# Optimization experiments

Measured on AMD Instinct MI355X. Metric: run time of the kernel, lower is better.

## Reference

```python
import jax, jax.numpy as jnp
import numpy as np

T, H, V = 2048, 2048, 32000
NH, NKV, DH = 16, 4, 128
E, K, I = 16, 2, 1024
EPS = 1e-6
THETA = 1000000.0


def _rms(x, w):
    # RMSNorm with add_unit_offset: scale = (1 + w)
    v = jnp.mean(x * x, axis=-1, keepdims=True)
    return x * jax.lax.rsqrt(v + EPS) * (1.0 + w)


def _rope(x, pos):
    # x: [T, heads, DH], neox-style rotate-half RoPE
    inv = 1.0 / (THETA ** (jnp.arange(0, DH, 2, dtype=jnp.float32) / DH))
    ang = pos.astype(jnp.float32)[:, None] * inv[None, :]  # [T, DH/2]
    c, s = jnp.cos(ang)[:, None, :], jnp.sin(ang)[:, None, :]
    x1, x2 = x[..., : DH // 2], x[..., DH // 2 :]
    return jnp.concatenate([x1 * c - x2 * s, x2 * c + x1 * s], axis=-1)


def setup_inputs():
    key = jax.random.key(0)
    ks = jax.random.split(key, 12)

    def n(k, shp, scale=0.02):
        return jax.random.normal(k, shp, dtype=jnp.float32) * scale

    return {
        "input_ids": jax.random.randint(ks[0], (T,), 0, V),
        "positions": jnp.arange(T),
        "hidden_states": jax.random.normal(ks[1], (T, H), dtype=jnp.float32),
        "spec_step_idx": 0,
        "embed_w": n(ks[2], (V, H)),
        "fc_w": n(ks[3], (2 * H, H)),
        "pre_fc_emb_w": jnp.zeros((H,), jnp.float32),
        "pre_fc_hid_w": jnp.zeros((H,), jnp.float32),
        "in_ln_w": jnp.zeros((H,), jnp.float32),
        "post_ln_w": jnp.zeros((H,), jnp.float32),
        "final_norm_w": jnp.zeros((H,), jnp.float32),
        "wq": n(ks[4], (H, NH * DH)),
        "wk": n(ks[5], (H, NKV * DH)),
        "wv": n(ks[6], (H, NKV * DH)),
        "wo": n(ks[7], (NH * DH, H)),
        "q_norm_w": jnp.zeros((DH,), jnp.float32),
        "k_norm_w": jnp.zeros((DH,), jnp.float32),
        "router_w": n(ks[8], (H, E)),
        "w_gate": n(ks[9], (E, H, I)),
        "w_up": n(ks[10], (E, H, I)),
        "w_down": n(ks[11], (E, I, H)),
    }


def reference(input_ids, positions, hidden_states, spec_step_idx, embed_w, fc_w,
              pre_fc_emb_w, pre_fc_hid_w, in_ln_w, post_ln_w, final_norm_w,
              wq, wk, wv, wo, q_norm_w, k_norm_w, router_w, w_gate, w_up, w_down):
    # 1-3. embed -> pre_fc norms -> concat -> fc (2H -> H, no bias)
    emb = _rms(embed_w[input_ids], pre_fc_emb_w)
    hid = _rms(hidden_states, pre_fc_hid_w)
    x = jnp.concatenate([emb, hid], axis=-1) @ fc_w  # [T, H]

    # 4. decoder layer (layer_idx = spec_step_idx % 1 == 0); vLLM fused add-RMSNorm residual pattern
    residual = x
    x = _rms(x, in_ln_w)

    # GQA attention with per-head q/k RMSNorm + RoPE, causal
    q = _rms((x @ wq).reshape(T, NH, DH), q_norm_w)
    k = _rms((x @ wk).reshape(T, NKV, DH), k_norm_w)
    v = (x @ wv).reshape(T, NKV, DH)
    q, k = _rope(q, positions), _rope(k, positions)
    rep = NH // NKV
    k, v = jnp.repeat(k, rep, axis=1), jnp.repeat(v, rep, axis=1)  # [T, NH, DH]
    scores = jnp.einsum("qhd,khd->hqk", q, k) * (DH ** -0.5)
    causal = positions[:, None] >= positions[None, :]
    scores = jnp.where(causal[None], scores, jnp.float32(-1e30))
    attn = jax.nn.softmax(scores, axis=-1)
    x = jnp.einsum("hqk,khd->qhd", attn, v).reshape(T, NH * DH) @ wo

    # post-attention norm with fused residual add
    x = x + residual
    residual = x
    x = _rms(x, post_ln_w)

    # MoE: softmax router, top-k renormalized, SwiGLU experts (dense weighted combine)
    probs = jax.nn.softmax(x @ router_w, axis=-1)  # [T, E]
    topv, topi = jax.lax.top_k(probs, K)
    topv = topv / jnp.sum(topv, axis=-1, keepdims=True)
    gates = jnp.zeros((T, E), x.dtype).at[jnp.arange(T)[:, None], topi].set(topv)
    g = jnp.einsum("th,ehi->tei", x, w_gate)
    u = jnp.einsum("th,ehi->tei", x, w_up)
    a = jax.nn.silu(g) * u  # [T, E, I]
    x = jnp.einsum("tei,eih,te->th", a, w_down, gates)

    # 5. final norm with residual add
    return _rms(x + residual, final_norm_w)
```

## Files before the change

### kernel.cpp

```cpp
#include <hip/hip_runtime.h>
#include <cstddef>


typedef unsigned short u16b;
typedef __attribute__((ext_vector_type(8))) short s8v;
typedef __attribute__((ext_vector_type(4))) float f4v;

#define T_TOK 2048
#define HID   2048

__device__ __forceinline__ float bf2f(u16b h) {
  return __uint_as_float(((unsigned int)h) << 16);
}
__device__ __forceinline__ u16b f2bf(float f) {
  unsigned int u = __float_as_uint(f);
  return (u16b)((u + 0x7fffu + ((u >> 16) & 1u)) >> 16);
}
__device__ __forceinline__ void split2(float f, u16b& hi, u16b& lo) {
  hi = f2bf(f);
  lo = f2bf(f - bf2f(hi));
}
__device__ __forceinline__ unsigned long long pack4(const u16b* p) {
  return (unsigned long long)p[0] | ((unsigned long long)p[1] << 16) |
         ((unsigned long long)p[2] << 32) | ((unsigned long long)p[3] << 48);
}
__device__ __forceinline__ f4v mfma_b(s8v a, s8v b, f4v c) {
  return __builtin_amdgcn_mfma_f32_16x16x32_bf16(a, b, c, 0, 0, 0);
}
union FragCvt { unsigned long long q[2]; s8v v; };

__device__ __forceinline__ float blk_sum_256(float v, float* lds4) {
  #pragma unroll
  for (int off = 32; off > 0; off >>= 1) v += __shfl_down(v, off);
  int tid = threadIdx.x;
  if ((tid & 63) == 0) lds4[tid >> 6] = v;
  __syncthreads();
  return lds4[0] + lds4[1] + lds4[2] + lds4[3];
}

__global__ void zero_counts_kernel(int* counts) {
  if (threadIdx.x < 16) counts[threadIdx.x] = 0;
}

__global__ __launch_bounds__(256) void embed_cat_kernel(
    const int* __restrict__ ids, const float* __restrict__ embw,
    const float* __restrict__ hid, const float* __restrict__ w_emb,
    const float* __restrict__ w_hid, u16b* __restrict__ catp) {
  __shared__ float lds[4];
  int t = blockIdx.x, which = blockIdx.y, tid = threadIdx.x;
  const float* src;
  const float* w;
  if (which == 0) { src = embw + (size_t)ids[t] * HID; w = w_emb; }
  else            { src = hid  + (size_t)t * HID;      w = w_hid; }
  u16b* dst = catp + (size_t)t * 8192 + which * 2048;
  float v[8]; float ss = 0.f;
  #pragma unroll
  for (int i = 0; i < 8; ++i) { v[i] = src[tid + i * 256]; ss += v[i] * v[i]; }
  float tot = blk_sum_256(ss, lds);
  float scale = rsqrtf(tot * (1.f / (float)HID) + 1e-6f);
  #pragma unroll
  for (int i = 0; i < 8; ++i) {
    int j = tid + i * 256;
    float val = v[i] * scale * (1.f + w[j]);
    u16b h, l;
    split2(val, h, l);
    dst[j] = h;
    dst[4096 + j] = l;
  }
}

__global__ __launch_bounds__(256) void rms_f32_kernel(
    const float* __restrict__ X, const float* __restrict__ W, float* __restrict__ Y) {
  __shared__ float lds[4];
  int t = blockIdx.x, tid = threadIdx.x;
  const float* row = X + (size_t)t * HID;
  float v[8]; float ss = 0.f;
  #pragma unroll
  for (int i = 0; i < 8; ++i) { v[i] = row[tid + i * 256]; ss += v[i] * v[i]; }
  float tot = blk_sum_256(ss, lds);
  float scale = rsqrtf(tot * (1.f / (float)HID) + 1e-6f);
  float* yrow = Y + (size_t)t * HID;
  #pragma unroll
  for (int i = 0; i < 8; ++i) {
    int j = tid + i * 256;
    yrow[j] = v[i] * scale * (1.f + W[j]);
  }
}

__global__ __launch_bounds__(256) void rms_split_kernel(
    const float* __restrict__ X, const float* __restrict__ W, u16b* __restrict__ Yp) {
  __shared__ float lds[4];
  int t = blockIdx.x, tid = threadIdx.x;
  const float* row = X + (size_t)t * HID;
  float v[8]; float ss = 0.f;
  #pragma unroll
  for (int i = 0; i < 8; ++i) { v[i] = row[tid + i * 256]; ss += v[i] * v[i]; }
  float tot = blk_sum_256(ss, lds);
  float scale = rsqrtf(tot * (1.f / (float)HID) + 1e-6f);
  u16b* yrow = Yp + (size_t)t * (2 * HID);
  #pragma unroll
  for (int i = 0; i < 8; ++i) {
    int j = tid + i * 256;
    float val = v[i] * scale * (1.f + W[j]);
    u16b h, l;
    split2(val, h, l);
    yrow[j] = h;
    yrow[HID + j] = l;
  }
}

__global__ __launch_bounds__(256) void tsplit_kernel(
    const float* __restrict__ B, u16b* __restrict__ Bt,
    int Kf, int N, int row_off) {
  __shared__ u16b ht[64][68];
  __shared__ u16b lt[64][68];
  int n0 = blockIdx.x * 64, k0 = blockIdx.y * 64;
  int tid = threadIdx.x;
  int kl = tid >> 4, nl = (tid & 15) * 4;
  #pragma unroll
  for (int p = 0; p < 4; ++p) {
    int kk = p * 16 + kl;
    float4 f = *(const float4*)&B[(size_t)(k0 + kk) * N + n0 + nl];
    float ff[4] = {f.x, f.y, f.z, f.w};
    #pragma unroll
    for (int j = 0; j < 4; ++j) {
      u16b h, l;
      split2(ff[j], h, l);
      ht[nl + j][kk] = h;
      lt[nl + j][kk] = l;
    }
  }
  __syncthreads();
  int ldo = 2 * Kf;
  int nr = tid >> 2, kc = (tid & 3) * 16;
  u16b* orow = Bt + (size_t)(row_off + n0 + nr) * ldo + k0 + kc;
  #pragma unroll
  for (int c = 0; c < 4; ++c) {
    *(unsigned long long*)(orow + c * 4)      = *(const unsigned long long*)&ht[nr][kc + c * 4];
    *(unsigned long long*)(orow + Kf + c * 4) = *(const unsigned long long*)&lt[nr][kc + c * 4];
  }
}

template <int EP>
__global__ __launch_bounds__(256) void gemm_bs(
    const u16b* __restrict__ Ap, const u16b* __restrict__ Bp,
    float* __restrict__ C, const float* __restrict__ addend,
    float* __restrict__ kout, float* __restrict__ vtout,
    int M, int N, int Kf) {
  __shared__ __attribute__((aligned(16))) u16b Ahs[64 * 40];
  __shared__ __attribute__((aligned(16))) u16b Als[64 * 40];
  __shared__ __attribute__((aligned(16))) u16b Bhs[64 * 40];
  __shared__ __attribute__((aligned(16))) u16b Bls[64 * 40];
  int n0 = blockIdx.x * 64, m0 = blockIdx.y * 64;
  int tid = threadIdx.x;
  int wave = tid >> 6, lane = tid & 63;
  int wm = wave >> 1, wn = wave & 1;
  int l16 = lane & 15, quad = lane >> 4;
  int lda = 2 * Kf;
  int sr = tid >> 2, skc = (tid & 3) * 8;
  const u16b* apH = Ap + (size_t)(m0 + sr) * lda + skc;
  const u16b* bpH = Bp + (size_t)(n0 + sr) * lda + skc;
  int sb = sr * 40 + skc;

  f4v acc[2][2];
  #pragma unroll
  for (int i = 0; i < 2; ++i)
    #pragma unroll
    for (int j = 0; j < 2; ++j) acc[i][j] = (f4v)0.0f;

  for (int k0 = 0; k0 < Kf; k0 += 32) {
    s8v ta = *(const s8v*)(apH + k0);
    s8v tb = *(const s8v*)(apH + Kf + k0);
    s8v tc = *(const s8v*)(bpH + k0);
    s8v td = *(const s8v*)(bpH + Kf + k0);
    __syncthreads();
    FragCvt u;
    u.v = ta;
    *(unsigned long long*)&Ahs[sb]     = u.q[0];
    *(unsigned long long*)&Ahs[sb + 4] = u.q[1];
    u.v = tb;
    *(unsigned long long*)&Als[sb]     = u.q[0];
    *(unsigned long long*)&Als[sb + 4] = u.q[1];
    u.v = tc;
    *(unsigned long long*)&Bhs[sb]     = u.q[0];
    *(unsigned long long*)&Bhs[sb + 4] = u.q[1];
    u.v = td;
    *(unsigned long long*)&Bls[sb]     = u.q[0];
    *(unsigned long long*)&Bls[sb + 4] = u.q[1];
    __syncthreads();
    s8v a0  = *(const s8v*)&Ahs[(wm * 32 + l16) * 40 + quad * 8];
    s8v a1  = *(const s8v*)&Ahs[(wm * 32 + 16 + l16) * 40 + quad * 8];
    s8v b0  = *(const s8v*)&Bhs[(wn * 32 + l16) * 40 + quad * 8];
    s8v b1  = *(const s8v*)&Bhs[(wn * 32 + 16 + l16) * 40 + quad * 8];
    s8v a0l = *(const s8v*)&Als[(wm * 32 + l16) * 40 + quad * 8];
    s8v a1l = *(const s8v*)&Als[(wm * 32 + 16 + l16) * 40 + quad * 8];
    s8v b0l = *(const s8v*)&Bls[(wn * 32 + l16) * 40 + quad * 8];
    s8v b1l = *(const s8v*)&Bls[(wn * 32 + 16 + l16) * 40 + quad * 8];
    acc[0][0] = mfma_b(a0, b0, acc[0][0]);
    acc[0][1] = mfma_b(a0, b1, acc[0][1]);
    acc[1][0] = mfma_b(a1, b0, acc[1][0]);
    acc[1][1] = mfma_b(a1, b1, acc[1][1]);
    acc[0][0] = mfma_b(a0, b0l, acc[0][0]);
    acc[0][1] = mfma_b(a0, b1l, acc[0][1]);
    acc[1][0] = mfma_b(a1, b0l, acc[1][0]);
    acc[1][1] = mfma_b(a1, b1l, acc[1][1]);
    acc[0][0] = mfma_b(a0l, b0, acc[0][0]);
    acc[0][1] = mfma_b(a0l, b1, acc[0][1]);
    acc[1][0] = mfma_b(a1l, b0, acc[1][0]);
    acc[1][1] = mfma_b(a1l, b1, acc[1][1]);
  }

  if (EP == 0) {
    #pragma unroll
    for (int i = 0; i < 2; ++i)
      #pragma unroll
      for (int j = 0; j < 2; ++j)
        #pragma unroll
        for (int r = 0; r < 4; ++r) {
          int mrow = m0 + wm * 32 + i * 16 + quad * 4 + r;
          int col = n0 + wn * 32 + j * 16 + l16;
          size_t idx = (size_t)mrow * N + col;
          C[idx] = acc[i][j][r] + (addend ? addend[idx] : 0.0f);
        }
  } else {
    if (n0 < 2048) {
      #pragma unroll
      for (int i = 0; i < 2; ++i)
        #pragma unroll
        for (int j = 0; j < 2; ++j)
          #pragma unroll
          for (int r = 0; r < 4; ++r) {
            int mrow = m0 + wm * 32 + i * 16 + quad * 4 + r;
            int col = n0 + wn * 32 + j * 16 + l16;
            C[(size_t)mrow * 2048 + col] = acc[i][j][r];
          }
    } else if (n0 < 2560) {
      #pragma unroll
      for (int i = 0; i < 2; ++i)
        #pragma unroll
        for (int j = 0; j < 2; ++j)
          #pragma unroll
          for (int r = 0; r < 4; ++r) {
            int mrow = m0 + wm * 32 + i * 16 + quad * 4 + r;
            int col = n0 + wn * 32 + j * 16 + l16 - 2048;
            kout[(size_t)mrow * 512 + col] = acc[i][j][r];
          }
    } else {
      #pragma unroll
      for (int i = 0; i < 2; ++i)
        #pragma unroll
        for (int j = 0; j < 2; ++j) {
          int vrow = n0 + wn * 32 + j * 16 + l16 - 2560;
          int mbase = m0 + wm * 32 + i * 16 + quad * 4;
          float4 vv;
          vv.x = acc[i][j][0]; vv.y = acc[i][j][1];
          vv.z = acc[i][j][2]; vv.w = acc[i][j][3];
          *(float4*)&vtout[(size_t)vrow * 2048 + mbase] = vv;
        }
    }
  }
}

__global__ __launch_bounds__(128) void qknorm_rope_kernel(
    float* __restrict__ X, const float* __restrict__ W,
    const int* __restrict__ positions, int ld) {
  __shared__ float wsum[2];
  __shared__ float xs[128];
  __shared__ float sc;
  int t = blockIdx.x, hh = blockIdx.y, d = threadIdx.x;
  float* row = X + (size_t)t * ld + hh * 128;
  float x = row[d];
  float ss = x * x;
  #pragma unroll
  for (int off = 32; off > 0; off >>= 1) ss += __shfl_down(ss, off);
  if ((d & 63) == 0) wsum[d >> 6] = ss;
  __syncthreads();
  if (d == 0) sc = rsqrtf((wsum[0] + wsum[1]) * (1.f / 128.f) + 1e-6f);
  __syncthreads();
  float xn = x * sc * (1.f + W[d]);
  xs[d] = xn;
  __syncthreads();
  int pos = positions[t];
  int i = d & 63;
  float invf = exp2f((float)i * (-19.931568569324174f / 64.f));
  float ang = (float)pos * invf;
  float cv = cosf(ang), sv = sinf(ang);
  float other = xs[d ^ 64];
  row[d] = (d < 64) ? (xn * cv - other * sv) : (xn * cv + other * sv);
}

template <int MODE>
__global__ __launch_bounds__(256) void gemm_k(
    const float* __restrict__ A, const float* __restrict__ B,
    const float* __restrict__ B2, float* __restrict__ C,
    const float* __restrict__ addend, const int* __restrict__ counts,
    const int* __restrict__ list, const float* __restrict__ gatebuf,
    int M, int N, int K) {
  __shared__ u16b As[64 * 40];
  __shared__ u16b Bs[64 * 40];
  __shared__ u16b B2s[64 * 40];

  int n0 = blockIdx.x * 64;
  int m0 = blockIdx.y * 64;
  int e = blockIdx.z;
  int cnt = counts[e];
  if (m0 >= cnt) return;
  list += e * T_TOK;
  B += (size_t)e * K * N;
  if (MODE == 1) B2 += (size_t)e * K * N;

  int tid = threadIdx.x;
  int wave = tid >> 6, lane = tid & 63;
  int wm = wave >> 1, wn = wave & 1;
  int l16 = lane & 15, quad = lane >> 4;

  int am = tid >> 2, ak = (tid & 3) * 8;
  int bk = tid >> 3, bn = (tid & 7) * 8;

  const float* aptr;
  {
    int mr = m0 + am;
    if (mr > cnt - 1) mr = cnt - 1;
    int entry = list[mr];
    int arow = (MODE == 1) ? (entry >> 1) : entry;
    aptr = A + (size_t)arow * K + ak;
  }
  const float* bptr = B + (size_t)bk * N + n0 + bn;
  const float* b2ptr = nullptr;
  if (MODE == 1) b2ptr = B2 + (size_t)bk * N + n0 + bn;

  f4v acc[2][2];
  f4v acc2[2][2];
  #pragma unroll
  for (int i = 0; i < 2; ++i)
    #pragma unroll
    for (int j = 0; j < 2; ++j) { acc[i][j] = (f4v)0.0f; acc2[i][j] = (f4v)0.0f; }

  for (int k0 = 0; k0 < K; k0 += 32) {
    __syncthreads();
    {
      const float* ap = aptr + k0;
      float4 f0 = *(const float4*)ap;
      float4 f1 = *(const float4*)(ap + 4);
      float f[8] = {f0.x, f0.y, f0.z, f0.w, f1.x, f1.y, f1.z, f1.w};
      u16b hi[8];
      #pragma unroll
      for (int x = 0; x < 8; ++x) hi[x] = f2bf(f[x]);
      *(unsigned long long*)&As[am * 40 + ak]     = pack4(hi);
      *(unsigned long long*)&As[am * 40 + ak + 4] = pack4(hi + 4);
    }
    {
      const float* bp = bptr + (size_t)k0 * N;
      float4 g0 = *(const float4*)bp;
      float4 g1 = *(const float4*)(bp + 4);
      float f[8] = {g0.x, g0.y, g0.z, g0.w, g1.x, g1.y, g1.z, g1.w};
      #pragma unroll
      for (int x = 0; x < 8; ++x) Bs[(bn + x) * 40 + bk] = f2bf(f[x]);
      if (MODE == 1) {
        const float* cp = b2ptr + (size_t)k0 * N;
        float4 h0 = *(const float4*)cp;
        float4 h1 = *(const float4*)(cp + 4);
        float f2[8] = {h0.x, h0.y, h0.z, h0.w, h1.x, h1.y, h1.z, h1.w};
        #pragma unroll
        for (int x = 0; x < 8; ++x) B2s[(bn + x) * 40 + bk] = f2bf(f2[x]);
      }
    }
    __syncthreads();
    s8v a0 = *(const s8v*)&As[(wm * 32 + l16) * 40 + quad * 8];
    s8v a1 = *(const s8v*)&As[(wm * 32 + 16 + l16) * 40 + quad * 8];
    s8v b0 = *(const s8v*)&Bs[(wn * 32 + l16) * 40 + quad * 8];
    s8v b1 = *(const s8v*)&Bs[(wn * 32 + 16 + l16) * 40 + quad * 8];
    acc[0][0] = mfma_b(a0, b0, acc[0][0]);
    acc[0][1] = mfma_b(a0, b1, acc[0][1]);
    acc[1][0] = mfma_b(a1, b0, acc[1][0]);
    acc[1][1] = mfma_b(a1, b1, acc[1][1]);
    if (MODE == 1) {
      s8v c0 = *(const s8v*)&B2s[(wn * 32 + l16) * 40 + quad * 8];
      s8v c1 = *(const s8v*)&B2s[(wn * 32 + 16 + l16) * 40 + quad * 8];
      acc2[0][0] = mfma_b(a0, c0, acc2[0][0]);
      acc2[0][1] = mfma_b(a0, c1, acc2[0][1]);
      acc2[1][0] = mfma_b(a1, c0, acc2[1][0]);
      acc2[1][1] = mfma_b(a1, c1, acc2[1][1]);
    }
  }

  #pragma unroll
  for (int i = 0; i < 2; ++i)
    #pragma unroll
    for (int j = 0; j < 2; ++j)
      #pragma unroll
      for (int r = 0; r < 4; ++r) {
        int mrow = m0 + wm * 32 + i * 16 + quad * 4 + r;
        int col = n0 + wn * 32 + j * 16 + l16;
        float val = acc[i][j][r];
        if (mrow < cnt) {
          int slot = list[mrow];
          if (MODE == 1) {
            float uu = acc2[i][j][r];
            float hv = val / (1.0f + __expf(-val)) * uu;
            C[(size_t)slot * N + col] = hv;
          } else {
            C[(size_t)slot * N + col] = val * gatebuf[slot];
          }
        }
      }
}

__global__ __launch_bounds__(256) void flash_kernel(
    const float* __restrict__ Q, const float* __restrict__ Kb,
    const float* __restrict__ VbT, u16b* __restrict__ attnp) {
  __shared__ __attribute__((aligned(16))) u16b Khi[32 * 136];
  __shared__ __attribute__((aligned(16))) u16b Klo[32 * 136];
  __shared__ __attribute__((aligned(16))) u16b Vthi[128 * 40];
  __shared__ __attribute__((aligned(16))) u16b Vtlo[128 * 40];
  __shared__ float Ss[32 * 36];
  __shared__ __attribute__((aligned(16))) u16b Phi[32 * 40];
  __shared__ __attribute__((aligned(16))) u16b Plo[32 * 40];
  __shared__ float red[32 * 8];
  __shared__ float mrow[32], lrow[32], arow[32];

  int qt = (gridDim.x - 1) - blockIdx.x;
  int h = blockIdx.y;
  int g = h >> 2;
  int tid = threadIdx.x;
  int wave = tid >> 6, lane = tid & 63;
  int l16 = lane & 15, quad = lane >> 4;
  int sm = wave >> 1, sn = wave & 1;

  s8v qhi[4], qlo[4];
  {
    const float* qp = Q + (size_t)(qt * 32 + sm * 16 + l16) * 2048 + h * 128 + quad * 8;
    #pragma unroll
    for (int kc = 0; kc < 4; ++kc) {
      float4 f0 = *(const float4*)(qp + kc * 32);
      float4 f1 = *(const float4*)(qp + kc * 32 + 4);
      float f[8] = {f0.x, f0.y, f0.z, f0.w, f1.x, f1.y, f1.z, f1.w};
      u16b hi[8], lo[8];
      #pragma unroll
      for (int x = 0; x < 8; ++x) split2(f[x], hi[x], lo[x]);
      FragCvt ch, cl;
      ch.q[0] = pack4(hi); ch.q[1] = pack4(hi + 4);
      cl.q[0] = pack4(lo); cl.q[1] = pack4(lo + 4);
      qhi[kc] = ch.v; qlo[kc] = cl.v;
    }
  }

  if (tid < 32) { mrow[tid] = -1e30f; lrow[tid] = 0.f; }

  f4v o[4];
  #pragma unroll
  for (int db = 0; db < 4; ++db) o[db] = (f4v)0.0f;

  int krow = tid >> 3, ksk = (tid & 7) * 16;
  int vd = tid >> 1, vk0 = (tid & 1) * 16;
  int sr = tid >> 3, sp = tid & 7;

  const u16b* krow_h = &Khi[(sn * 16 + l16) * 136];
  const u16b* krow_l = &Klo[(sn * 16 + l16) * 136];

  for (int kt = 0; kt <= qt; ++kt) {
    __syncthreads();
    {
      const float* ks = Kb + (size_t)(kt * 32 + krow) * 512 + g * 128 + ksk;
      int kb = krow * 136 + ksk;
      #pragma unroll
      for (int half = 0; half < 2; ++half) {
        float4 f0 = *(const float4*)(ks + half * 8);
        float4 f1 = *(const float4*)(ks + half * 8 + 4);
        float f[8] = {f0.x, f0.y, f0.z, f0.w, f1.x, f1.y, f1.z, f1.w};
        u16b hi[8], lo[8];
        #pragma unroll
        for (int x = 0; x < 8; ++x) split2(f[x], hi[x], lo[x]);
        *(unsigned long long*)&Khi[kb + half * 8]     = pack4(hi);
        *(unsigned long long*)&Khi[kb + half * 8 + 4] = pack4(hi + 4);
        *(unsigned long long*)&Klo[kb + half * 8]     = pack4(lo);
        *(unsigned long long*)&Klo[kb + half * 8 + 4] = pack4(lo + 4);
      }
      const float* vs = VbT + (size_t)(g * 128 + vd) * 2048 + kt * 32 + vk0;
      int vb = vd * 40 + vk0;
      #pragma unroll
      for (int half = 0; half < 2; ++half) {
        float4 f0 = *(const float4*)(vs + half * 8);
        float4 f1 = *(const float4*)(vs + half * 8 + 4);
        float f[8] = {f0.x, f0.y, f0.z, f0.w, f1.x, f1.y, f1.z, f1.w};
        u16b hi[8], lo[8];
        #pragma unroll
        for (int x = 0; x < 8; ++x) split2(f[x], hi[x], lo[x]);
        *(unsigned long long*)&Vthi[vb + half * 8]     = pack4(hi);
        *(unsigned long long*)&Vthi[vb + half * 8 + 4] = pack4(hi + 4);
        *(unsigned long long*)&Vtlo[vb + half * 8]     = pack4(lo);
        *(unsigned long long*)&Vtlo[vb + half * 8 + 4] = pack4(lo + 4);
      }
    }
    __syncthreads();
    f4v a0 = (f4v)0.0f, a1 = (f4v)0.0f, a2 = (f4v)0.0f;
    __builtin_amdgcn_s_setprio(1);
    #pragma unroll
    for (int kc = 0; kc < 4; ++kc) {
      s8v kh = *(const s8v*)(krow_h + kc * 32 + quad * 8);
      s8v kl = *(const s8v*)(krow_l + kc * 32 + quad * 8);
      a0 = mfma_b(qhi[kc], kh, a0);
      a1 = mfma_b(qhi[kc], kl, a1);
      a2 = mfma_b(qlo[kc], kh, a2);
    }
    __builtin_amdgcn_s_setprio(0);
    {
      f4v sacc = a0 + a1 + a2;
      const float sc = 0.08838834764831845f;
      #pragma unroll
      for (int r = 0; r < 4; ++r) {
        int row_l = sm * 16 + quad * 4 + r;
        int col_l = sn * 16 + l16;
        int qb = qt * 32 + row_l, kb2 = kt * 32 + col_l;
        Ss[row_l * 36 + col_l] = (kb2 <= qb) ? sacc[r] * sc : -1e30f;
      }
    }
    __syncthreads();
    float mx = -3e38f;
    #pragma unroll
    for (int c = sp * 4; c < sp * 4 + 4; ++c) mx = fmaxf(mx, Ss[sr * 36 + c]);
    red[sr * 8 + sp] = mx;
    __syncthreads();
    if (sp == 0) {
      float mn = mrow[sr];
      #pragma unroll
      for (int p = 0; p < 8; ++p) mn = fmaxf(mn, red[sr * 8 + p]);
      arow[sr] = __expf(mrow[sr] - mn);
      mrow[sr] = mn;
    }
    __syncthreads();
    {
      float m = mrow[sr];
      float sum = 0.f;
      #pragma unroll
      for (int c = sp * 4; c < sp * 4 + 4; ++c) {
        float e2 = __expf(Ss[sr * 36 + c] - m);
        u16b eh, el;
        split2(e2, eh, el);
        Phi[sr * 40 + c] = eh;
        Plo[sr * 40 + c] = el;
        sum += e2;
      }
      red[sr * 8 + sp] = sum;
    }
    __syncthreads();
    if (sp == 0) {
      float s2 = 0.f;
      #pragma unroll
      for (int p = 0; p < 8; ++p) s2 += red[sr * 8 + p];
      lrow[sr] = lrow[sr] * arow[sr] + s2;
    }
    {
      f4v arv;
      arv[0] = arow[sm * 16 + quad * 4 + 0];
      arv[1] = arow[sm * 16 + quad * 4 + 1];
      arv[2] = arow[sm * 16 + quad * 4 + 2];
      arv[3] = arow[sm * 16 + quad * 4 + 3];
      #pragma unroll
      for (int db = 0; db < 4; ++db) o[db] *= arv;

      s8v pah = *(const s8v*)&Phi[(sm * 16 + l16) * 40 + quad * 8];
      s8v pal = *(const s8v*)&Plo[(sm * 16 + l16) * 40 + quad * 8];
      __builtin_amdgcn_s_setprio(1);
      #pragma unroll
      for (int db = 0; db < 4; ++db) {
        int vrow = sn * 64 + db * 16 + l16;
        s8v vh = *(const s8v*)&Vthi[vrow * 40 + quad * 8];
        s8v vl = *(const s8v*)&Vtlo[vrow * 40 + quad * 8];
        o[db] = mfma_b(pah, vh, o[db]);
        o[db] = mfma_b(pah, vl, o[db]);
        o[db] = mfma_b(pal, vh, o[db]);
      }
      __builtin_amdgcn_s_setprio(0);
    }
  }
  __syncthreads();
  {
    int row0 = sm * 16 + quad * 4;
    f4v invv;
    invv[0] = 1.f / lrow[row0 + 0];
    invv[1] = 1.f / lrow[row0 + 1];
    invv[2] = 1.f / lrow[row0 + 2];
    invv[3] = 1.f / lrow[row0 + 3];
    #pragma unroll
    for (int db = 0; db < 4; ++db) o[db] *= invv;
    #pragma unroll
    for (int r = 0; r < 4; ++r) {
      u16b* ob = attnp + (size_t)(qt * 32 + row0 + r) * 4096 + h * 128 + sn * 64 + l16;
      #pragma unroll
      for (int db = 0; db < 4; ++db) {
        u16b hh, ll;
        split2(o[db][r], hh, ll);
        ob[db * 16] = hh;
        ob[2048 + db * 16] = ll;
      }
    }
  }
}

__global__ __launch_bounds__(256) void router_kernel(
    const float* __restrict__ xn2, const float* __restrict__ rw,
    int* __restrict__ counts, int* __restrict__ list, float* __restrict__ gatebuf) {
  __shared__ float red[256];
  __shared__ float logits[16];
  int t = blockIdx.x, tid = threadIdx.x;
  int e = tid >> 4, p = tid & 15;
  const float* xr = xn2 + (size_t)t * HID;
  float s = 0.f;
  for (int j = p * 128; j < p * 128 + 128; ++j) s += xr[j] * rw[j * 16 + e];
  red[tid] = s;
  __syncthreads();
  if (tid < 16) {
    float l = 0.f;
    #pragma unroll
    for (int p2 = 0; p2 < 16; ++p2) l += red[tid * 16 + p2];
    logits[tid] = l;
  }
  __syncthreads();
  if (tid == 0) {
    int i0 = 0; float l0 = logits[0];
    for (int i = 1; i < 16; ++i) if (logits[i] > l0) { l0 = logits[i]; i0 = i; }
    int i1 = -1; float l1 = -3e38f;
    for (int i = 0; i < 16; ++i) if (i != i0 && logits[i] > l1) { l1 = logits[i]; i1 = i; }
    float g0 = 1.f / (1.f + __expf(l1 - l0));
    float g1 = 1.f - g0;
    int s0 = atomicAdd(&counts[i0], 1);
    list[i0 * T_TOK + s0] = t * 2;
    gatebuf[t * 2] = g0;
    int s1 = atomicAdd(&counts[i1], 1);
    list[i1 * T_TOK + s1] = t * 2 + 1;
    gatebuf[t * 2 + 1] = g1;
  }
}

__global__ __launch_bounds__(256) void final_kernel(
    const float* __restrict__ moeout, const float* __restrict__ resid,
    const float* __restrict__ W, float* __restrict__ out) {
  __shared__ float lds[4];
  int t = blockIdx.x, tid = threadIdx.x;
  const float* m0 = moeout + (size_t)(2 * t) * HID;
  const float* m1 = moeout + (size_t)(2 * t + 1) * HID;
  const float* rr = resid + (size_t)t * HID;
  float v[8]; float ss = 0.f;
  #pragma unroll
  for (int i = 0; i < 8; ++i) {
    int j = tid + i * 256;
    v[i] = m0[j] + m1[j] + rr[j];
    ss += v[i] * v[i];
  }
  float tot = blk_sum_256(ss, lds);
  float scale = rsqrtf(tot * (1.f / (float)HID) + 1e-6f);
  float* orow = out + (size_t)t * HID;
  #pragma unroll
  for (int i = 0; i < 8; ++i) {
    int j = tid + i * 256;
    orow[j] = v[i] * scale * (1.f + W[j]);
  }
}

extern "C" void kernel_launch(void* const* d_in, const int* in_sizes, int n_in,
                              void* d_out, int out_size, void* d_ws, size_t ws_size,
                              hipStream_t stream) {
  const int* input_ids   = (const int*)d_in[0];
  const int* positions   = (const int*)d_in[1];
  const float* hidden    = (const float*)d_in[2];
  const float* embed_w   = (const float*)d_in[4];
  const float* fc_w      = (const float*)d_in[5];
  const float* pre_emb   = (const float*)d_in[6];
  const float* pre_hid   = (const float*)d_in[7];
  const float* in_ln     = (const float*)d_in[8];
  const float* post_ln   = (const float*)d_in[9];
  const float* final_w   = (const float*)d_in[10];
  const float* wq        = (const float*)d_in[11];
  const float* wk        = (const float*)d_in[12];
  const float* wv        = (const float*)d_in[13];
  const float* wo        = (const float*)d_in[14];
  const float* qnw       = (const float*)d_in[15];
  const float* knw       = (const float*)d_in[16];
  const float* rw        = (const float*)d_in[17];
  const float* wg        = (const float*)d_in[18];
  const float* wu        = (const float*)d_in[19];
  const float* wd        = (const float*)d_in[20];

  char* ws = (char*)d_ws;
  u16b*  catp   = (u16b*)(ws + 0);
  u16b*  qkvw   = (u16b*)(ws + 0);
  float* moeout = (float*)(ws + 0);
  float* x      = (float*)(ws + 33554432);
  u16b*  xnp    = (u16b*)(ws + 50331648);
  u16b*  wotw   = (u16b*)(ws + 50331648);
  float* q      = (float*)(ws + 67108864);
  float* kbuf   = (float*)(ws + 83886080);
  float* vbufT  = (float*)(ws + 88080384);
  u16b*  fctw   = (u16b*)(ws + 92274688);
  u16b*  attnp  = (u16b*)(ws + 92274688);
  float* x2     = (float*)(ws + 109051904);
  float* xn2    = (float*)(ws + 125829120);
  int*   counts = (int*)(ws + 142606336);
  int*   list   = (int*)(ws + 142606592);
  float* gateb  = (float*)(ws + 142737664);
  float* hbuf   = q;

  zero_counts_kernel<<<1, 64, 0, stream>>>(counts);
  embed_cat_kernel<<<dim3(2048, 2), 256, 0, stream>>>(input_ids, embed_w, hidden,
                                                      pre_emb, pre_hid, catp);
  tsplit_kernel<<<dim3(32, 64), 256, 0, stream>>>(fc_w, fctw, 4096, 2048, 0);
  gemm_bs<0><<<dim3(32, 32), 256, 0, stream>>>(catp, fctw, x, nullptr,
                                               nullptr, nullptr, 2048, 2048, 4096);
  tsplit_kernel<<<dim3(32, 32), 256, 0, stream>>>(wq, qkvw, 2048, 2048, 0);
  tsplit_kernel<<<dim3(8, 32), 256, 0, stream>>>(wk, qkvw, 2048, 512, 2048);
  tsplit_kernel<<<dim3(8, 32), 256, 0, stream>>>(wv, qkvw, 2048, 512, 2560);
  rms_split_kernel<<<2048, 256, 0, stream>>>(x, in_ln, xnp);
  gemm_bs<1><<<dim3(48, 32), 256, 0, stream>>>(xnp, qkvw, q, nullptr,
                                               kbuf, vbufT, 2048, 3072, 2048);
  tsplit_kernel<<<dim3(32, 32), 256, 0, stream>>>(wo, wotw, 2048, 2048, 0);
  qknorm_rope_kernel<<<dim3(2048, 16), 128, 0, stream>>>(q, qnw, positions, 2048);
  qknorm_rope_kernel<<<dim3(2048, 4), 128, 0, stream>>>(kbuf, knw, positions, 512);
  flash_kernel<<<dim3(64, 16), 256, 0, stream>>>(q, kbuf, vbufT, attnp);
  gemm_bs<0><<<dim3(32, 32), 256, 0, stream>>>(attnp, wotw, x2, x,
                                               nullptr, nullptr, 2048, 2048, 2048);
  rms_f32_kernel<<<2048, 256, 0, stream>>>(x2, post_ln, xn2);
  router_kernel<<<2048, 256, 0, stream>>>(xn2, rw, counts, list, gateb);
  gemm_k<1><<<dim3(16, 32, 16), 256, 0, stream>>>(xn2, wg, wu, hbuf, nullptr,
                                                  counts, list, nullptr, 0, 1024, 2048);
  gemm_k<2><<<dim3(32, 32, 16), 256, 0, stream>>>(hbuf, wd, nullptr, moeout, nullptr,
                                                  counts, list, gateb, 0, 2048, 1024);
  final_kernel<<<2048, 256, 0, stream>>>(moeout, x2, final_w, (float*)d_out);
}
```

Baseline: 1.714 ms.

## Rewrite MoE GEMMs with 128-row tiles, bf16 activations, and swizzled LDS

Result: faster. 1.541 ms (-10.1%).

```diff
diff --git a/kernel.cpp b/kernel.cpp
--- a/kernel.cpp
+++ b/kernel.cpp
@@ -290,18 +290,18 @@
 }
 
 template <int MODE>
-__global__ __launch_bounds__(256) void gemm_k(
-    const float* __restrict__ A, const float* __restrict__ B,
-    const float* __restrict__ B2, float* __restrict__ C,
-    const float* __restrict__ addend, const int* __restrict__ counts,
-    const int* __restrict__ list, const float* __restrict__ gatebuf,
-    int M, int N, int K) {
-  __shared__ u16b As[64 * 40];
-  __shared__ u16b Bs[64 * 40];
-  __shared__ u16b B2s[64 * 40];
+__global__ __launch_bounds__(256) void gemm_moe(
+    const u16b* __restrict__ Ap, int lda,
+    const float* __restrict__ B, const float* __restrict__ B2,
+    u16b* __restrict__ hout, float* __restrict__ moeout,
+    const int* __restrict__ counts, const int* __restrict__ list,
+    const float* __restrict__ gatebuf, int N, int K) {
+  __shared__ __attribute__((aligned(16))) u16b As[128 * 40];
+  __shared__ __attribute__((aligned(16))) u16b Bs[64 * 40];
+  __shared__ __attribute__((aligned(16))) u16b B2s[(MODE == 1) ? 64 * 40 : 8];
 
   int n0 = blockIdx.x * 64;
-  int m0 = blockIdx.y * 64;
+  int m0 = blockIdx.y * 128;
   int e = blockIdx.z;
   int cnt = counts[e];
   if (m0 >= cnt) return;
@@ -314,93 +314,101 @@
   int wm = wave >> 1, wn = wave & 1;
   int l16 = lane & 15, quad = lane >> 4;
 
-  int am = tid >> 2, ak = (tid & 3) * 8;
-  int bk = tid >> 3, bn = (tid & 7) * 8;
-
-  const float* aptr;
+  int ar = tid >> 1, ac0 = (tid & 1) * 2;
+  int axr = (ar >> 3) & 3;
+  const u16b* aptr;
   {
-    int mr = m0 + am;
+    int mr = m0 + ar;
     if (mr > cnt - 1) mr = cnt - 1;
     int entry = list[mr];
     int arow = (MODE == 1) ? (entry >> 1) : entry;
-    aptr = A + (size_t)arow * K + ak;
-  }
-  const float* bptr = B + (size_t)bk * N + n0 + bn;
+    aptr = Ap + (size_t)arow * lda;
+  }
+  int bk = tid >> 3, bn8 = (tid & 7) * 8;
+  const float* bptr = B + (size_t)bk * N + n0 + bn8;
   const float* b2ptr = nullptr;
-  if (MODE == 1) b2ptr = B2 + (size_t)bk * N + n0 + bn;
-
-  f4v acc[2][2];
-  f4v acc2[2][2];
-  #pragma unroll
-  for (int i = 0; i < 2; ++i)
+  if (MODE == 1) b2ptr = B2 + (size_t)bk * N + n0 + bn8;
+  int bcol = (bk >> 3) * 8 + (bk & 7);
+
+  f4v acc[4][2];
+  f4v acc2[4][2];
+  #pragma unroll
+  for (int i = 0; i < 4; ++i)
     #pragma unroll
     for (int j = 0; j < 2; ++j) { acc[i][j] = (f4v)0.0f; acc2[i][j] = (f4v)0.0f; }
 
   for (int k0 = 0; k0 < K; k0 += 32) {
-    __syncthreads();
+    s8v ta0 = *(const s8v*)(aptr + k0 + ac0 * 8);
+    s8v ta1 = *(const s8v*)(aptr + k0 + ac0 * 8 + 8);
+    float4 g0 = *(const float4*)(bptr + (size_t)k0 * N);
+    float4 g1 = *(const float4*)(bptr + (size_t)k0 * N + 4);
+    float4 h0, h1;
+    if (MODE == 1) {
+      h0 = *(const float4*)(b2ptr + (size_t)k0 * N);
+      h1 = *(const float4*)(b2ptr + (size_t)k0 * N + 4);
+    }
+    __syncthreads();
+    *(s8v*)&As[ar * 40 + ((ac0 ^ axr) * 8)]       = ta0;
+    *(s8v*)&As[ar * 40 + (((ac0 + 1) ^ axr) * 8)] = ta1;
     {
-      const float* ap = aptr + k0;
-      float4 f0 = *(const float4*)ap;
-      float4 f1 = *(const float4*)(ap + 4);
-      float f[8] = {f0.x, f0.y, f0.z, f0.w, f1.x, f1.y, f1.z, f1.w};
-      u16b hi[8];
-      #pragma unroll
-      for (int x = 0; x < 8; ++x) hi[x] = f2bf(f[x]);
-      *(unsigned long long*)&As[am * 40 + ak]     = pack4(hi);
-      *(unsigned long long*)&As[am * 40 + ak + 4] = pack4(hi + 4);
-    }
-    {
-      const float* bp = bptr + (size_t)k0 * N;
-      float4 g0 = *(const float4*)bp;
-      float4 g1 = *(const float4*)(bp + 4);
       float f[8] = {g0.x, g0.y, g0.z, g0.w, g1.x, g1.y, g1.z, g1.w};
       #pragma unroll
-      for (int x = 0; x < 8; ++x) Bs[(bn + x) * 40 + bk] = f2bf(f[x]);
+      for (int x = 0; x < 8; ++x) {
+        int n = bn8 + x;
+        int col = ((bk >> 3) ^ ((n >> 3) & 3)) * 8 + (bk & 7);
+        Bs[n * 40 + col] = f2bf(f[x]);
+      }
       if (MODE == 1) {
-        const float* cp = b2ptr + (size_t)k0 * N;
-        float4 h0 = *(const float4*)cp;
-        float4 h1 = *(const float4*)(cp + 4);
         float f2[8] = {h0.x, h0.y, h0.z, h0.w, h1.x, h1.y, h1.z, h1.w};
         #pragma unroll
-        for (int x = 0; x < 8; ++x) B2s[(bn + x) * 40 + bk] = f2bf(f2[x]);
-      }
-    }
-    __syncthreads();
-    s8v a0 = *(const s8v*)&As[(wm * 32 + l16) * 40 + quad * 8];
-    s8v a1 = *(const s8v*)&As[(wm * 32 + 16 + l16) * 40 + quad * 8];
-    s8v b0 = *(const s8v*)&Bs[(wn * 32 + l16) * 40 + quad * 8];
-    s8v b1 = *(const s8v*)&Bs[(wn * 32 + 16 + l16) * 40 + quad * 8];
-    acc[0][0] = mfma_b(a0, b0, acc[0][0]);
-    acc[0][1] = mfma_b(a0, b1, acc[0][1]);
-    acc[1][0] = mfma_b(a1, b0, acc[1][0]);
-    acc[1][1] = mfma_b(a1, b1, acc[1][1]);
-    if (MODE == 1) {
-      s8v c0 = *(const s8v*)&B2s[(wn * 32 + l16) * 40 + quad * 8];
-      s8v c1 = *(const s8v*)&B2s[(wn * 32 + 16 + l16) * 40 + quad * 8];
-      acc2[0][0] = mfma_b(a0, c0, acc2[0][0]);
-      acc2[0][1] = mfma_b(a0, c1, acc2[0][1]);
-      acc2[1][0] = mfma_b(a1, c0, acc2[1][0]);
-      acc2[1][1] = mfma_b(a1, c1, acc2[1][1]);
-    }
-  }
-
-  #pragma unroll
-  for (int i = 0; i < 2; ++i)
+        for (int x = 0; x < 8; ++x) {
+          int n = bn8 + x;
+          int col = ((bk >> 3) ^ ((n >> 3) & 3)) * 8 + (bk & 7);
+          B2s[n * 40 + col] = f2bf(f2[x]);
+        }
+      }
+    }
+    __syncthreads();
+    s8v a[4], b[2], c2[2];
+    #pragma unroll
+    for (int i = 0; i < 4; ++i) {
+      int row = wm * 64 + i * 16 + l16;
+      a[i] = *(const s8v*)&As[row * 40 + ((quad ^ ((row >> 3) & 3)) * 8)];
+    }
+    #pragma unroll
+    for (int j = 0; j < 2; ++j) {
+      int row = wn * 32 + j * 16 + l16;
+      b[j] = *(const s8v*)&Bs[row * 40 + ((quad ^ ((row >> 3) & 3)) * 8)];
+      if (MODE == 1)
+        c2[j] = *(const s8v*)&B2s[row * 40 + ((quad ^ ((row >> 3) & 3)) * 8)];
+    }
+    __builtin_amdgcn_s_setprio(1);
+    #pragma unroll
+    for (int i = 0; i < 4; ++i)
+      #pragma unroll
+      for (int j = 0; j < 2; ++j) {
+        acc[i][j] = mfma_b(a[i], b[j], acc[i][j]);
+        if (MODE == 1) acc2[i][j] = mfma_b(a[i], c2[j], acc2[i][j]);
+      }
+    __builtin_amdgcn_s_setprio(0);
+  }
+
+  #pragma unroll
+  for (int i = 0; i < 4; ++i)
     #pragma unroll
     for (int j = 0; j < 2; ++j)
       #pragma unroll
       for (int r = 0; r < 4; ++r) {
-        int mrow = m0 + wm * 32 + i * 16 + quad * 4 + r;
-        int col = n0 + wn * 32 + j * 16 + l16;
-        float val = acc[i][j][r];
+        int mrow = m0 + wm * 64 + i * 16 + quad * 4 + r;
         if (mrow < cnt) {
           int slot = list[mrow];
+          int col = n0 + wn * 32 + j * 16 + l16;
           if (MODE == 1) {
-            float uu = acc2[i][j][r];
-            float hv = val / (1.0f + __expf(-val)) * uu;
-            C[(size_t)slot * N + col] = hv;
+            float g = acc[i][j][r], u = acc2[i][j][r];
+            float hv = g / (1.0f + __expf(-g)) * u;
+            hout[(size_t)slot * N + col] = f2bf(hv);
           } else {
-            C[(size_t)slot * N + col] = val * gatebuf[slot];
+            moeout[(size_t)slot * N + col] = acc[i][j][r] * gatebuf[slot];
           }
         }
       }
@@ -690,6 +698,7 @@
   u16b*  xnp    = (u16b*)(ws + 50331648);
   u16b*  wotw   = (u16b*)(ws + 50331648);
   float* q      = (float*)(ws + 67108864);
+  u16b*  hbuf16 = (u16b*)(ws + 67108864);
   float* kbuf   = (float*)(ws + 83886080);
   float* vbufT  = (float*)(ws + 88080384);
   u16b*  fctw   = (u16b*)(ws + 92274688);
@@ -699,7 +708,6 @@
   int*   counts = (int*)(ws + 142606336);
   int*   list   = (int*)(ws + 142606592);
   float* gateb  = (float*)(ws + 142737664);
-  float* hbuf   = q;
 
   zero_counts_kernel<<<1, 64, 0, stream>>>(counts);
   embed_cat_kernel<<<dim3(2048, 2), 256, 0, stream>>>(input_ids, embed_w, hidden,
@@ -720,10 +728,13 @@
   gemm_bs<0><<<dim3(32, 32), 256, 0, stream>>>(attnp, wotw, x2, x,
                                                nullptr, nullptr, 2048, 2048, 2048);
   rms_f32_kernel<<<2048, 256, 0, stream>>>(x2, post_ln, xn2);
+  rms_split_kernel<<<2048, 256, 0, stream>>>(x2, post_ln, xnp);
   router_kernel<<<2048, 256, 0, stream>>>(xn2, rw, counts, list, gateb);
-  gemm_k<1><<<dim3(16, 32, 16), 256, 0, stream>>>(xn2, wg, wu, hbuf, nullptr,
-                                                  counts, list, nullptr, 0, 1024, 2048);
-  gemm_k<2><<<dim3(32, 32, 16), 256, 0, stream>>>(hbuf, wd, nullptr, moeout, nullptr,
-                                                  counts, list, gateb, 0, 2048, 1024);
+  gemm_moe<1><<<dim3(16, 16, 16), 256, 0, stream>>>(xnp, 4096, wg, wu, hbuf16,
+                                                    nullptr, counts, list, nullptr,
+                                                    1024, 2048);
+  gemm_moe<2><<<dim3(32, 16, 16), 256, 0, stream>>>(hbuf16, 1024, wd, nullptr, nullptr,
+                                                    moeout, counts, list, gateb,
+                                                    2048, 1024);
   final_kernel<<<2048, 256, 0, stream>>>(moeout, x2, final_w, (float*)d_out);
 }
```
